# Kernel optimization log

Measured on AMD Instinct MI355X. Metric: run time of the kernel, lower is better.

Reference implementation:

```python
import jax, jax.numpy as jnp
import numpy as np

B, L, H, P, A, T = 64, 256, 1024, 64, 512, 8


def setup_inputs() -> dict:
    key = jax.random.key(0)
    ks = jax.random.split(key, 9)
    return {
        "word_hiddens": jax.random.normal(ks[0], (B, L, H), dtype=jnp.float32),
        "pos_e1_embeddings": jax.random.normal(ks[1], (B, L, P), dtype=jnp.float32),
        "pos_e2_embeddings": jax.random.normal(ks[2], (B, L, P), dtype=jnp.float32),
        "e1_end": jax.random.randint(ks[3], (B,), 0, L, dtype=jnp.int32),
        "e2_end": jax.random.randint(ks[4], (B,), 0, L, dtype=jnp.int32),
        "type_embeddings": jax.random.normal(ks[5], (T, H), dtype=jnp.float32) * 0.03,
        "W_pos": jax.random.normal(ks[6], (H + 2 * P, A), dtype=jnp.float32) * 0.03,
        "W_ent": jax.random.normal(ks[7], (4 * H, A), dtype=jnp.float32) * 0.02,
        "v": jax.random.normal(ks[8], (A,), dtype=jnp.float32) * 0.05,
    }


def _latent_type(e_h, type_emb):
    # alpha = softmax(e_h @ C^T); latent type = alpha @ C   (C: [T, latent])
    scores = jnp.einsum("bh,th->bt", e_h, type_emb)
    alpha = jax.nn.softmax(scores, axis=-1)
    return jnp.einsum("bt,th->bh", alpha, type_emb)


def reference(word_hiddens, pos_e1_embeddings, pos_e2_embeddings, e1_end, e2_end,
              type_embeddings, W_pos, W_ent, v):
    b, seq_len, h = word_hiddens.shape
    batch_idx = jnp.arange(b)
    e1_h = word_hiddens[batch_idx, e1_end]          # [B, H]
    e2_h = word_hiddens[batch_idx, e2_end]          # [B, H]
    e1_type = _latent_type(e1_h, type_embeddings)   # [B, H]
    e2_type = _latent_type(e2_h, type_embeddings)   # [B, H]

    entity_features = jnp.concatenate([e1_h, e1_type, e2_h, e2_type], axis=-1)  # [B, 4H]
    pos_features = jnp.concatenate([word_hiddens, pos_e1_embeddings, pos_e2_embeddings], axis=-1)  # [B, L, H+2P]

    dense_pos = jnp.einsum("blf,fa->bla", pos_features, W_pos)   # [B, L, A]
    dense_ent = entity_features @ W_ent                          # [B, A]
    # Faithful to original tf.repeat(axis=1)+reshape (element-interleaved, not a broadcast)
    dense_ent_r = jnp.repeat(dense_ent, seq_len, axis=1).reshape(b, seq_len, -1)  # [B, L, A]

    u = jnp.tanh(dense_pos + dense_ent_r)            # [B, L, A]
    vu = jnp.einsum("bla,a->bl", u, v)               # [B, L]
    alpha = jax.nn.softmax(vu, axis=-1)              # [B, L]
    z = jnp.einsum("blh,bl->bh", word_hiddens, alpha)  # [B, H]
    return z
```

## Files before the change

### kernel.cpp

```cpp
#include <hip/hip_runtime.h>
#include <hip/hip_bf16.h>
#include <math.h>

#define B_ 64
#define L_ 256
#define H_ 1024
#define P_ 64
#define A_ 512
#define T_ 8
#define NSTEP 36

#define AS1 __attribute__((address_space(1)))
#define AS3 __attribute__((address_space(3)))

typedef __attribute__((ext_vector_type(8))) __bf16 bf16x8;
typedef __attribute__((ext_vector_type(4))) float f32x4;

__device__ __forceinline__ float bf2f(ushort u) {
  union { unsigned int i; float f; } v; v.i = ((unsigned int)u) << 16; return v.f;
}
__device__ __forceinline__ ushort f2bf_rne(float f) {
  union { float f; unsigned int i; } v; v.f = f;
  unsigned int r = v.i + 0x7FFFu + ((v.i >> 16) & 1u);
  return (ushort)(r >> 16);
}
__device__ __forceinline__ unsigned int pack2_rne(float a, float b) {
  return (unsigned int)f2bf_rne(a) | ((unsigned int)f2bf_rne(b) << 16);
}

template <bool BF16>
__device__ __forceinline__ float ld1(const void* p, size_t i) {
  if (BF16) return bf2f(((const ushort*)p)[i]);
  return ((const float*)p)[i];
}
template <bool BF16>
__device__ __forceinline__ float2 ld2(const void* p, size_t i) {
  if (BF16) {
    ushort2 u = *(const ushort2*)((const ushort*)p + i);
    return (float2){bf2f(u.x), bf2f(u.y)};
  }
  return *(const float2*)((const float*)p + i);
}
template <bool BF16>
__device__ __forceinline__ float4 ld4(const void* p, size_t i) {
  if (BF16) {
    ushort4 u = *(const ushort4*)((const ushort*)p + i);
    return (float4){bf2f(u.x), bf2f(u.y), bf2f(u.z), bf2f(u.w)};
  }
  return *(const float4*)((const float*)p + i);
}

__device__ __forceinline__ void gll16(const void* g, void* l) {
  __builtin_amdgcn_global_load_lds((const AS1 void*)g, (AS3 void*)l, 16, 0, 0);
}

__device__ __forceinline__ void bar_vm2() {
  __builtin_amdgcn_sched_barrier(0);
  asm volatile("s_waitcnt vmcnt(2) lgkmcnt(0)" ::: "memory");
  __builtin_amdgcn_sched_barrier(0);
  __builtin_amdgcn_s_barrier();
  __builtin_amdgcn_sched_barrier(0);
}
__device__ __forceinline__ void bar_vm0() {
  __builtin_amdgcn_sched_barrier(0);
  asm volatile("s_waitcnt vmcnt(0) lgkmcnt(0)" ::: "memory");
  __builtin_amdgcn_sched_barrier(0);
  __builtin_amdgcn_s_barrier();
  __builtin_amdgcn_sched_barrier(0);
}

template <bool BF16>
__global__ __launch_bounds__(256) void prep_k(
    const void* __restrict__ wpos, ushort* __restrict__ WTs,
    const void* __restrict__ wh, const int* __restrict__ e1e,
    const int* __restrict__ e2e, const void* __restrict__ temb,
    float* __restrict__ EF) {
  if (blockIdx.x < 576) {
    __shared__ ushort tile[32][33];
    const int s  = blockIdx.x >> 4;
    const int at = blockIdx.x & 15;
    const int tx = threadIdx.x & 31;
    const int ty = threadIdx.x >> 5;
#pragma unroll
    for (int i = 0; i < 4; ++i) {
      size_t idx = (size_t)(s * 32 + ty + i * 8) * A_ + at * 32 + tx;
      ushort u;
      if (BF16) u = ((const ushort*)wpos)[idx];
      else u = f2bf_rne(((const float*)wpos)[idx]);
      tile[ty + i * 8][tx] = u;
    }
    __syncthreads();
#pragma unroll
    for (int i = 0; i < 4; ++i) {
      WTs[(size_t)s * (A_ * 32) + (size_t)(at * 32 + ty + i * 8) * 32 + tx] =
          tile[tx][ty + i * 8];
    }
  } else {
    const int b = blockIdx.x - 576;
    const int tid = threadIdx.x;
    __shared__ float eh1[1024];
    __shared__ float eh2[1024];
    __shared__ float part[256][16];
    __shared__ float part2[16][17];
    __shared__ float scores[16];
    __shared__ float alpha[16];

    const size_t o1 = ((size_t)b * L_ + e1e[b]) * H_;
    const size_t o2 = ((size_t)b * L_ + e2e[b]) * H_;
    for (int h = tid; h < 1024; h += 256) {
      eh1[h] = ld1<BF16>(wh, o1 + h);
      eh2[h] = ld1<BF16>(wh, o2 + h);
    }
    __syncthreads();

    float p[16];
#pragma unroll
    for (int t = 0; t < 16; ++t) p[t] = 0.f;
    for (int h = tid; h < 1024; h += 256) {
      float a1 = eh1[h], a2 = eh2[h];
#pragma unroll
      for (int t = 0; t < 8; ++t) {
        float c = ld1<BF16>(temb, t * 1024 + h);
        p[t] += a1 * c;
        p[8 + t] += a2 * c;
      }
    }
#pragma unroll
    for (int t = 0; t < 16; ++t) part[tid][t] = p[t];
    __syncthreads();
    {
      const int t = tid & 15, j = tid >> 4;
      float s = 0.f;
#pragma unroll
      for (int i = 0; i < 16; ++i) s += part[j * 16 + i][t];
      part2[j][t] = s;
    }
    __syncthreads();
    if (tid < 16) {
      float s = 0.f;
#pragma unroll
      for (int i = 0; i < 16; ++i) s += part2[i][tid];
      scores[tid] = s;
    }
    __syncthreads();
    if (tid < 2) {
      const int base = tid * 8;
      float mx = scores[base];
      for (int t = 1; t < 8; ++t) mx = fmaxf(mx, scores[base + t]);
      float sum = 0.f;
      float e[8];
      for (int t = 0; t < 8; ++t) { e[t] = __expf(scores[base + t] - mx); sum += e[t]; }
      float inv = 1.f / sum;
      for (int t = 0; t < 8; ++t) alpha[base + t] = e[t] * inv;
    }
    __syncthreads();

    float* efb = EF + (size_t)b * 4096;
    for (int h = tid; h < 1024; h += 256) {
      float l1 = 0.f, l2 = 0.f;
#pragma unroll
      for (int t = 0; t < 8; ++t) {
        float c = ld1<BF16>(temb, t * 1024 + h);
        l1 += alpha[t] * c;
        l2 += alpha[8 + t] * c;
      }
      efb[h] = eh1[h];
      efb[1024 + h] = l1;
      efb[2048 + h] = eh2[h];
      efb[3072 + h] = l2;
    }
  }
}

template <bool BF16>
__global__ __launch_bounds__(256) void ent_gemm(const float* __restrict__ EF,
                                                const void* __restrict__ went,
                                                float* __restrict__ part) {
  const int mh = blockIdx.x & 1;
  const int nb = (blockIdx.x >> 1) & 3;
  const int kb = blockIdx.x >> 3;
  const int tid = threadIdx.x;
  __shared__ float efs[32][128];

  const int k0 = kb * 128;
  {
    const int kq = (tid & 31) * 4;
    for (int m = tid >> 5; m < 32; m += 8) {
      *(float4*)&efs[m][kq] = *(const float4*)&EF[(size_t)(mh * 32 + m) * 4096 + k0 + kq];
    }
  }
  __syncthreads();

  const int n0 = nb * 128 + (tid & 31) * 4;
  const int mg = (tid >> 5) * 4;
  float acc[4][4];
#pragma unroll
  for (int i = 0; i < 4; ++i)
#pragma unroll
    for (int j = 0; j < 4; ++j) acc[i][j] = 0.f;

  for (int k = 0; k < 128; ++k) {
    float4 w = ld4<BF16>(went, (size_t)(k0 + k) * A_ + n0);
#pragma unroll
    for (int i = 0; i < 4; ++i) {
      float e = efs[mg + i][k];
      acc[i][0] += e * w.x;
      acc[i][1] += e * w.y;
      acc[i][2] += e * w.z;
      acc[i][3] += e * w.w;
    }
  }
#pragma unroll
  for (int i = 0; i < 4; ++i) {
    *(float4*)&part[((size_t)kb * 64 + mh * 32 + mg + i) * A_ + n0] =
        (float4){acc[i][0], acc[i][1], acc[i][2], acc[i][3]};
  }
}

__global__ __launch_bounds__(256, 4) void fused_gemm_vu_bf16(
    const ushort* __restrict__ wh, const ushort* __restrict__ pe1,
    const ushort* __restrict__ pe2, const ushort* __restrict__ WTs,
    const float* __restrict__ part, const ushort* __restrict__ vvec,
    float* __restrict__ vu_part) {
  __shared__ __align__(16) ushort Abuf[2][2048];
  __shared__ __align__(16) ushort Bbuf[2][4096];
  __shared__ float vu_s[4][64];
  __shared__ float dense_s[64];

  const int tid = threadIdx.x;
  const int pid = blockIdx.x;
  const int wid = (pid & 7) * 128 + (pid >> 3);
  const int nb = wid & 3;
  const int mb = wid >> 2;
  const int rbase = mb * 64;
  const int wave = tid >> 6;
  const int lane = tid & 63;
  const int quad = lane >> 4;
  const int col = lane & 15;
  const int wr = wave >> 1;
  const int wc = wave & 1;

  int aoff[2], boff[4];
#pragma unroll
  for (int mf = 0; mf < 2; ++mf) {
    const int ra = wr * 32 + mf * 16 + col;
    aoff[mf] = ra * 32 + ((quad ^ ((ra >> 1) & 3)) << 3);
  }
#pragma unroll
  for (int nf = 0; nf < 4; ++nf) {
    const int rb = wc * 64 + nf * 16 + col;
    boff[nf] = rb * 32 + ((quad ^ ((rb >> 1) & 3)) << 3);
  }

  const int srow = tid >> 2;
  const int csw = (((tid & 3) ^ ((srow >> 1) & 3)) << 3);
  const ushort* aw  = wh  + (size_t)(rbase + srow) * H_ + csw;
  const ushort* ap1 = pe1 + (size_t)(rbase + srow) * P_ + csw;
  const ushort* ap2 = pe2 + (size_t)(rbase + srow) * P_ + csw;
  const ushort* b1  = WTs + (size_t)(nb * 128 + srow) * 32 + csw;
  const ushort* b2  = WTs + (size_t)(nb * 128 + 64 + srow) * 32 + csw;

  auto stage = [&](int buf, int s) {
    const ushort* as;
    if (s < 32)      as = aw + s * 32;
    else if (s < 34) as = ap1 + (s - 32) * 32;
    else             as = ap2 + (s - 34) * 32;
    const size_t so = (size_t)s * (A_ * 32);
    gll16(as, &Abuf[buf][wave * 512]);
    gll16(b1 + so, &Bbuf[buf][wave * 512]);
    gll16(b2 + so, &Bbuf[buf][2048 + wave * 512]);
  };

  f32x4 acc[2][4];
#pragma unroll
  for (int i = 0; i < 2; ++i)
#pragma unroll
    for (int j = 0; j < 4; ++j) acc[i][j] = (f32x4){0.f, 0.f, 0.f, 0.f};

  const int bidx = rbase >> 8;
  float de = 0.f;
  if (tid < 64) {
    const int a = 2 * ((rbase & 255) + tid) + (nb >> 1);
#pragma unroll
    for (int kb = 0; kb < 32; ++kb)
      de += part[((size_t)kb * 64 + bidx) * A_ + a];
  }
  stage(0, 0);
  if (tid < 64) dense_s[tid] = de;
  __syncthreads();

  int buf = 0;
  for (int s = 0; s < NSTEP; ++s) {
    if (s + 1 < NSTEP) stage(buf ^ 1, s + 1);
    const ushort* Ab = Abuf[buf];
    const ushort* Bb = Bbuf[buf];
    bf16x8 af[2], bfr[4];
#pragma unroll
    for (int mf = 0; mf < 2; ++mf) af[mf] = *(const bf16x8*)&Ab[aoff[mf]];
#pragma unroll
    for (int nf = 0; nf < 4; ++nf) bfr[nf] = *(const bf16x8*)&Bb[boff[nf]];
#pragma unroll
    for (int mf = 0; mf < 2; ++mf)
#pragma unroll
      for (int nf = 0; nf < 4; ++nf)
        acc[mf][nf] =
            __builtin_amdgcn_mfma_f32_16x16x32_bf16(af[mf], bfr[nf], acc[mf][nf], 0, 0, 0);
    __syncthreads();
    buf ^= 1;
  }

  float vv[4];
#pragma unroll
  for (int nf = 0; nf < 4; ++nf)
    vv[nf] = bf2f(vvec[nb * 128 + wc * 64 + nf * 16 + col]);

#pragma unroll
  for (int mf = 0; mf < 2; ++mf) {
    const int row0 = wr * 32 + mf * 16 + quad * 4;
    const float e0 = dense_s[row0 + 0];
    const float e1 = dense_s[row0 + 1];
    const float e2 = dense_s[row0 + 2];
    const float e3 = dense_s[row0 + 3];
    float s0 = 0.f, s1 = 0.f, s2 = 0.f, s3 = 0.f;
#pragma unroll
    for (int nf = 0; nf < 4; ++nf) {
      float vn = vv[nf];
      s0 += tanhf(acc[mf][nf][0] + e0) * vn;
      s1 += tanhf(acc[mf][nf][1] + e1) * vn;
      s2 += tanhf(acc[mf][nf][2] + e2) * vn;
      s3 += tanhf(acc[mf][nf][3] + e3) * vn;
    }
    s0 += __shfl_xor(s0, 1); s0 += __shfl_xor(s0, 2); s0 += __shfl_xor(s0, 4); s0 += __shfl_xor(s0, 8);
    s1 += __shfl_xor(s1, 1); s1 += __shfl_xor(s1, 2); s1 += __shfl_xor(s1, 4); s1 += __shfl_xor(s1, 8);
    s2 += __shfl_xor(s2, 1); s2 += __shfl_xor(s2, 2); s2 += __shfl_xor(s2, 4); s2 += __shfl_xor(s2, 8);
    s3 += __shfl_xor(s3, 1); s3 += __shfl_xor(s3, 2); s3 += __shfl_xor(s3, 4); s3 += __shfl_xor(s3, 8);
    if (col == 0) {
      vu_s[wave][row0 + 0] = s0;
      vu_s[wave][row0 + 1] = s1;
      vu_s[wave][row0 + 2] = s2;
      vu_s[wave][row0 + 3] = s3;
    }
  }
  __syncthreads();
  if (tid < 64) {
    const int wrr = tid >> 5;
    float s = vu_s[wrr * 2][tid] + vu_s[wrr * 2 + 1][tid];
    vu_part[(size_t)nb * (B_ * L_) + rbase + tid] = s;
  }
}

__global__ __launch_bounds__(256, 4) void fused_gemm_vu_f32(
    const float* __restrict__ wh, const float* __restrict__ pe1,
    const float* __restrict__ pe2, const ushort* __restrict__ WTs,
    const float* __restrict__ part, const float* __restrict__ vvec,
    float* __restrict__ vu_part) {
  __shared__ __align__(16) ushort Abuf[2][2048];
  __shared__ __align__(16) ushort Bbuf[2][4096];
  __shared__ float vu_s[4][64];
  __shared__ float dense_s[64];

  const int tid = threadIdx.x;
  const int pid = blockIdx.x;
  const int wid = (pid & 7) * 128 + (pid >> 3);
  const int nb = wid & 3;
  const int mb = wid >> 2;
  const int rbase = mb * 64;
  const int wave = tid >> 6;
  const int lane = tid & 63;
  const int quad = lane >> 4;
  const int col = lane & 15;
  const int wr = wave >> 1;
  const int wc = wave & 1;

  int aoff[2], boff[4];
#pragma unroll
  for (int mf = 0; mf < 2; ++mf) {
    const int ra = wr * 32 + mf * 16 + col;
    aoff[mf] = ra * 32 + ((quad ^ ((ra >> 1) & 3)) << 3);
  }
#pragma unroll
  for (int nf = 0; nf < 4; ++nf) {
    const int rb = wc * 64 + nf * 16 + col;
    boff[nf] = rb * 32 + ((quad ^ ((rb >> 1) & 3)) << 3);
  }

  const int srow = tid >> 2;
  const int csw = (((tid & 3) ^ ((srow >> 1) & 3)) << 3);
  const ushort* b1 = WTs + (size_t)(nb * 128 + srow) * 32 + csw;
  const ushort* b2 = WTs + (size_t)(nb * 128 + 64 + srow) * 32 + csw;
  auto gllB = [&](int buf, int s) {
    const size_t so = (size_t)s * (A_ * 32);
    gll16(b1 + so, &Bbuf[buf][wave * 512]);
    gll16(b2 + so, &Bbuf[buf][2048 + wave * 512]);
  };

  const int ar0 = tid >> 2, aq = tid & 3;
  const int sA0 = ar0 * 32 + ((aq ^ ((ar0 >> 1) & 3)) << 3);

  f32x4 acc[2][4];
#pragma unroll
  for (int i = 0; i < 2; ++i)
#pragma unroll
    for (int j = 0; j < 4; ++j) acc[i][j] = (f32x4){0.f, 0.f, 0.f, 0.f};

  float4 fXa, fXb;
  float4 fYa, fYb;

  auto ISSUE_X = [&](int s) {
    const float* src; int ld, k0;
    if (s < 32)      { src = wh;  ld = H_; k0 = s * 32; }
    else if (s < 34) { src = pe1; ld = P_; k0 = (s - 32) * 32; }
    else             { src = pe2; ld = P_; k0 = (s - 34) * 32; }
    const float* p0 = src + (size_t)(rbase + ar0) * ld + k0 + aq * 8;
    fXa = *(const float4*)p0;
    fXb = *(const float4*)(p0 + 4);
  };
  auto ISSUE_Y = [&](int s) {
    const float* src; int ld, k0;
    if (s < 32)      { src = wh;  ld = H_; k0 = s * 32; }
    else if (s < 34) { src = pe1; ld = P_; k0 = (s - 32) * 32; }
    else             { src = pe2; ld = P_; k0 = (s - 34) * 32; }
    const float* p0 = src + (size_t)(rbase + ar0) * ld + k0 + aq * 8;
    fYa = *(const float4*)p0;
    fYb = *(const float4*)(p0 + 4);
  };
  auto STORE_X = [&](int buf) {
    uint4 u0 = {pack2_rne(fXa.x, fXa.y), pack2_rne(fXa.z, fXa.w),
                pack2_rne(fXb.x, fXb.y), pack2_rne(fXb.z, fXb.w)};
    *(uint4*)&Abuf[buf][sA0] = u0;
  };
  auto STORE_Y = [&](int buf) {
    uint4 u0 = {pack2_rne(fYa.x, fYa.y), pack2_rne(fYa.z, fYa.w),
                pack2_rne(fYb.x, fYb.y), pack2_rne(fYb.z, fYb.w)};
    *(uint4*)&Abuf[buf][sA0] = u0;
  };
  auto COMPUTE = [&](int buf) {
    bf16x8 af[2], bfr[4];
#pragma unroll
    for (int mf = 0; mf < 2; ++mf) af[mf] = *(const bf16x8*)&Abuf[buf][aoff[mf]];
#pragma unroll
    for (int nf = 0; nf < 4; ++nf) bfr[nf] = *(const bf16x8*)&Bbuf[buf][boff[nf]];
#pragma unroll
    for (int mf = 0; mf < 2; ++mf)
#pragma unroll
      for (int nf = 0; nf < 4; ++nf)
        acc[mf][nf] =
            __builtin_amdgcn_mfma_f32_16x16x32_bf16(af[mf], bfr[nf], acc[mf][nf], 0, 0, 0);
  };

  const int bidx = rbase >> 8;
  float de = 0.f;
  if (tid < 64) {
    const int a = 2 * ((rbase & 255) + tid) + (nb >> 1);
#pragma unroll
    for (int kb = 0; kb < 32; ++kb)
      de += part[((size_t)kb * 64 + bidx) * A_ + a];
  }
  gllB(0, 0);
  ISSUE_X(0);
  ISSUE_Y(1);
  STORE_X(0);
  if (tid < 64) dense_s[tid] = de;
  __syncthreads();

  for (int s = 0; s < NSTEP; s += 2) {
    gllB(1, s + 1);
    __builtin_amdgcn_sched_barrier(0);
    if (s + 2 < NSTEP) ISSUE_X(s + 2);
    COMPUTE(0);
    STORE_Y(1);
    if (s + 2 < NSTEP) bar_vm2(); else bar_vm0();
    if (s + 2 < NSTEP) {
      gllB(0, s + 2);
      __builtin_amdgcn_sched_barrier(0);
      if (s + 3 < NSTEP) ISSUE_Y(s + 3);
    }
    COMPUTE(1);
    if (s + 2 < NSTEP) {
      STORE_X(0);
      if (s + 3 < NSTEP) bar_vm2(); else bar_vm0();
    }
  }

  float vv[4];
#pragma unroll
  for (int nf = 0; nf < 4; ++nf)
    vv[nf] = vvec[nb * 128 + wc * 64 + nf * 16 + col];

#pragma unroll
  for (int mf = 0; mf < 2; ++mf) {
    const int row0 = wr * 32 + mf * 16 + quad * 4;
    const float e0 = dense_s[row0 + 0];
    const float e1 = dense_s[row0 + 1];
    const float e2 = dense_s[row0 + 2];
    const float e3 = dense_s[row0 + 3];
    float s0 = 0.f, s1 = 0.f, s2 = 0.f, s3 = 0.f;
#pragma unroll
    for (int nf = 0; nf < 4; ++nf) {
      float vn = vv[nf];
      s0 += tanhf(acc[mf][nf][0] + e0) * vn;
      s1 += tanhf(acc[mf][nf][1] + e1) * vn;
      s2 += tanhf(acc[mf][nf][2] + e2) * vn;
      s3 += tanhf(acc[mf][nf][3] + e3) * vn;
    }
    s0 += __shfl_xor(s0, 1); s0 += __shfl_xor(s0, 2); s0 += __shfl_xor(s0, 4); s0 += __shfl_xor(s0, 8);
    s1 += __shfl_xor(s1, 1); s1 += __shfl_xor(s1, 2); s1 += __shfl_xor(s1, 4); s1 += __shfl_xor(s1, 8);
    s2 += __shfl_xor(s2, 1); s2 += __shfl_xor(s2, 2); s2 += __shfl_xor(s2, 4); s2 += __shfl_xor(s2, 8);
    s3 += __shfl_xor(s3, 1); s3 += __shfl_xor(s3, 2); s3 += __shfl_xor(s3, 4); s3 += __shfl_xor(s3, 8);
    if (col == 0) {
      vu_s[wave][row0 + 0] = s0;
      vu_s[wave][row0 + 1] = s1;
      vu_s[wave][row0 + 2] = s2;
      vu_s[wave][row0 + 3] = s3;
    }
  }
  __syncthreads();
  if (tid < 64) {
    const int wrr = tid >> 5;
    float s = vu_s[wrr * 2][tid] + vu_s[wrr * 2 + 1][tid];
    vu_part[(size_t)nb * (B_ * L_) + rbase + tid] = s;
  }
}

template <bool BF16>
__global__ __launch_bounds__(256) void softmax_z(const void* __restrict__ wh,
                                                 const float* __restrict__ vu_part,
                                                 void* __restrict__ out) {
  const int b = blockIdx.x >> 1;
  const int hh = blockIdx.x & 1;
  const int tid = threadIdx.x;
  __shared__ float alpha[256];
  __shared__ float red[256];

  float x = 0.f;
#pragma unroll
  for (int p = 0; p < 4; ++p) x += vu_part[(size_t)p * (B_ * L_) + b * L_ + tid];
  red[tid] = x;
  __syncthreads();
  for (int s = 128; s > 0; s >>= 1) {
    if (tid < s) red[tid] = fmaxf(red[tid], red[tid + s]);
    __syncthreads();
  }
  float m = red[0];
  __syncthreads();
  float e = __expf(x - m);
  red[tid] = e;
  __syncthreads();
  for (int s = 128; s > 0; s >>= 1) {
    if (tid < s) red[tid] += red[tid + s];
    __syncthreads();
  }
  alpha[tid] = e / red[0];
  __syncthreads();

  const int h0 = hh * 512 + tid * 2;
  const size_t base = (size_t)b * L_ * H_ + h0;
  float z0 = 0.f, z1 = 0.f;
  for (int l = 0; l < 256; l += 8) {
    float2 u0 = ld2<BF16>(wh, base + (size_t)(l + 0) * H_);
    float2 u1 = ld2<BF16>(wh, base + (size_t)(l + 1) * H_);
    float2 u2 = ld2<BF16>(wh, base + (size_t)(l + 2) * H_);
    float2 u3 = ld2<BF16>(wh, base + (size_t)(l + 3) * H_);
    float2 u4 = ld2<BF16>(wh, base + (size_t)(l + 4) * H_);
    float2 u5 = ld2<BF16>(wh, base + (size_t)(l + 5) * H_);
    float2 u6 = ld2<BF16>(wh, base + (size_t)(l + 6) * H_);
    float2 u7 = ld2<BF16>(wh, base + (size_t)(l + 7) * H_);
    float a0 = alpha[l + 0], a1 = alpha[l + 1], a2 = alpha[l + 2], a3 = alpha[l + 3];
    float a4 = alpha[l + 4], a5 = alpha[l + 5], a6 = alpha[l + 6], a7 = alpha[l + 7];
    z0 += a0 * u0.x + a1 * u1.x + a2 * u2.x + a3 * u3.x
        + a4 * u4.x + a5 * u5.x + a6 * u6.x + a7 * u7.x;
    z1 += a0 * u0.y + a1 * u1.y + a2 * u2.y + a3 * u3.y
        + a4 * u4.y + a5 * u5.y + a6 * u6.y + a7 * u7.y;
  }
  if (BF16) {
    ((unsigned int*)out)[((size_t)b * H_ + h0) >> 1] = pack2_rne(z0, z1);
  } else {
    *(float2*)((float*)out + (size_t)b * H_ + h0) = (float2){z0, z1};
  }
}

extern "C" void kernel_launch(void* const* d_in, const int* in_sizes, int n_in,
                              void* d_out, int out_size, void* d_ws, size_t ws_size,
                              hipStream_t stream) {
  const void* wh   = d_in[0];
  const void* pe1  = d_in[1];
  const void* pe2  = d_in[2];
  const int*  e1e  = (const int*)d_in[3];
  const int*  e2e  = (const int*)d_in[4];
  const void* temb = d_in[5];
  const void* wpos = d_in[6];
  const void* went = d_in[7];
  const void* vvec = d_in[8];

  const bool bf16 = (in_sizes[0] == (int)(B_ * L_ * H_ * 2));

  char* ws = (char*)d_ws;
  ushort* WTs      = (ushort*)ws;
  float* vu_part   = (float*)(ws + 1310720);
  float* EF        = (float*)(ws + 1310720);
  float* part      = (float*)(ws + 2359296);

  if (bf16) {
    prep_k<true ><<<dim3(640), dim3(256), 0, stream>>>(wpos, WTs, wh, e1e, e2e, temb, EF);
    ent_gemm<true ><<<dim3(256), dim3(256), 0, stream>>>(EF, went, part);
    fused_gemm_vu_bf16<<<dim3(1024), dim3(256), 0, stream>>>(
        (const ushort*)wh, (const ushort*)pe1, (const ushort*)pe2, WTs, part,
        (const ushort*)vvec, vu_part);
    softmax_z<true ><<<dim3(128), dim3(256), 0, stream>>>(wh, vu_part, d_out);
  } else {
    prep_k<false><<<dim3(640), dim3(256), 0, stream>>>(wpos, WTs, wh, e1e, e2e, temb, EF);
    ent_gemm<false><<<dim3(256), dim3(256), 0, stream>>>(EF, went, part);
    fused_gemm_vu_f32<<<dim3(1024), dim3(256), 0, stream>>>(
        (const float*)wh, (const float*)pe1, (const float*)pe2, WTs, part,
        (const float*)vvec, vu_part);
    softmax_z<false><<<dim3(128), dim3(256), 0, stream>>>(wh, vu_part, d_out);
  }
}
```

Before: 187.1 us.

## Deepen fused GEMM pipeline to triple-buffered LDS with two-stage prefetch

Changes the fused GEMM + tanh/vu kernel's K-loop from double to triple buffering of the A and B LDS tiles. Global loads now run two stages ahead of compute, with vmcnt(6) waits in place of vmcnt(2). The aim is to hide more global memory latency behind the MFMA work. In exchange it uses more LDS and more registers for the extra prefetched A fragments, which could lower occupancy under the launch bound of 4 blocks.

```diff
diff --git a/kernel.cpp b/kernel.cpp
--- a/kernel.cpp
+++ b/kernel.cpp
@@ -54,19 +54,28 @@
   __builtin_amdgcn_global_load_lds((const AS1 void*)g, (AS3 void*)l, 16, 0, 0);
 }
 
-__device__ __forceinline__ void bar_vm2() {
-  __builtin_amdgcn_sched_barrier(0);
-  asm volatile("s_waitcnt vmcnt(2) lgkmcnt(0)" ::: "memory");
-  __builtin_amdgcn_sched_barrier(0);
+__device__ __forceinline__ void SB() { __builtin_amdgcn_sched_barrier(0); }
+
+__device__ __forceinline__ void bar_vm6() {
+  SB();
+  asm volatile("s_waitcnt vmcnt(6) lgkmcnt(0)" ::: "memory");
+  SB();
   __builtin_amdgcn_s_barrier();
-  __builtin_amdgcn_sched_barrier(0);
+  SB();
+}
+__device__ __forceinline__ void bar_vm4() {
+  SB();
+  asm volatile("s_waitcnt vmcnt(4) lgkmcnt(0)" ::: "memory");
+  SB();
+  __builtin_amdgcn_s_barrier();
+  SB();
 }
 __device__ __forceinline__ void bar_vm0() {
-  __builtin_amdgcn_sched_barrier(0);
+  SB();
   asm volatile("s_waitcnt vmcnt(0) lgkmcnt(0)" ::: "memory");
-  __builtin_amdgcn_sched_barrier(0);
+  SB();
   __builtin_amdgcn_s_barrier();
-  __builtin_amdgcn_sched_barrier(0);
+  SB();
 }
 
 template <bool BF16>
@@ -354,8 +363,8 @@
     const float* __restrict__ pe2, const ushort* __restrict__ WTs,
     const float* __restrict__ part, const float* __restrict__ vvec,
     float* __restrict__ vu_part) {
-  __shared__ __align__(16) ushort Abuf[2][2048];
-  __shared__ __align__(16) ushort Bbuf[2][4096];
+  __shared__ __align__(16) ushort Abuf[3][2048];
+  __shared__ __align__(16) ushort Bbuf[3][4096];
   __shared__ float vu_s[4][64];
   __shared__ float dense_s[64];
 
@@ -396,6 +405,35 @@
 
   const int ar0 = tid >> 2, aq = tid & 3;
   const int sA0 = ar0 * 32 + ((aq ^ ((ar0 >> 1) & 3)) << 3);
+  const float* asrc_w  = wh  + (size_t)(rbase + ar0) * H_ + aq * 8;
+  const float* asrc_p1 = pe1 + (size_t)(rbase + ar0) * P_ + aq * 8;
+  const float* asrc_p2 = pe2 + (size_t)(rbase + ar0) * P_ + aq * 8;
+
+  float4 fA0a, fA0b, fA1a, fA1b, fA2a, fA2b;
+
+  auto aptr = [&](int s) -> const float* {
+    if (s < 32) return asrc_w + s * 32;
+    if (s < 34) return asrc_p1 + (s - 32) * 32;
+    return asrc_p2 + (s - 34) * 32;
+  };
+  auto issue0 = [&](int s) { const float* p = aptr(s); fA0a = *(const float4*)p; fA0b = *(const float4*)(p + 4); };
+  auto issue1 = [&](int s) { const float* p = aptr(s); fA1a = *(const float4*)p; fA1b = *(const float4*)(p + 4); };
+  auto issue2 = [&](int s) { const float* p = aptr(s); fA2a = *(const float4*)p; fA2b = *(const float4*)(p + 4); };
+  auto store0 = [&](int buf) {
+    uint4 u = {pack2_rne(fA0a.x, fA0a.y), pack2_rne(fA0a.z, fA0a.w),
+               pack2_rne(fA0b.x, fA0b.y), pack2_rne(fA0b.z, fA0b.w)};
+    *(uint4*)&Abuf[buf][sA0] = u;
+  };
+  auto store1 = [&](int buf) {
+    uint4 u = {pack2_rne(fA1a.x, fA1a.y), pack2_rne(fA1a.z, fA1a.w),
+               pack2_rne(fA1b.x, fA1b.y), pack2_rne(fA1b.z, fA1b.w)};
+    *(uint4*)&Abuf[buf][sA0] = u;
+  };
+  auto store2 = [&](int buf) {
+    uint4 u = {pack2_rne(fA2a.x, fA2a.y), pack2_rne(fA2a.z, fA2a.w),
+               pack2_rne(fA2b.x, fA2b.y), pack2_rne(fA2b.z, fA2b.w)};
+    *(uint4*)&Abuf[buf][sA0] = u;
+  };
 
   f32x4 acc[2][4];
 #pragma unroll
@@ -403,37 +441,6 @@
 #pragma unroll
     for (int j = 0; j < 4; ++j) acc[i][j] = (f32x4){0.f, 0.f, 0.f, 0.f};
 
-  float4 fXa, fXb;
-  float4 fYa, fYb;
-
-  auto ISSUE_X = [&](int s) {
-    const float* src; int ld, k0;
-    if (s < 32)      { src = wh;  ld = H_; k0 = s * 32; }
-    else if (s < 34) { src = pe1; ld = P_; k0 = (s - 32) * 32; }
-    else             { src = pe2; ld = P_; k0 = (s - 34) * 32; }
-    const float* p0 = src + (size_t)(rbase + ar0) * ld + k0 + aq * 8;
-    fXa = *(const float4*)p0;
-    fXb = *(const float4*)(p0 + 4);
-  };
-  auto ISSUE_Y = [&](int s) {
-    const float* src; int ld, k0;
-    if (s < 32)      { src = wh;  ld = H_; k0 = s * 32; }
-    else if (s < 34) { src = pe1; ld = P_; k0 = (s - 32) * 32; }
-    else             { src = pe2; ld = P_; k0 = (s - 34) * 32; }
-    const float* p0 = src + (size_t)(rbase + ar0) * ld + k0 + aq * 8;
-    fYa = *(const float4*)p0;
-    fYb = *(const float4*)(p0 + 4);
-  };
-  auto STORE_X = [&](int buf) {
-    uint4 u0 = {pack2_rne(fXa.x, fXa.y), pack2_rne(fXa.z, fXa.w),
-                pack2_rne(fXb.x, fXb.y), pack2_rne(fXb.z, fXb.w)};
-    *(uint4*)&Abuf[buf][sA0] = u0;
-  };
-  auto STORE_Y = [&](int buf) {
-    uint4 u0 = {pack2_rne(fYa.x, fYa.y), pack2_rne(fYa.z, fYa.w),
-                pack2_rne(fYb.x, fYb.y), pack2_rne(fYb.z, fYb.w)};
-    *(uint4*)&Abuf[buf][sA0] = u0;
-  };
   auto COMPUTE = [&](int buf) {
     bf16x8 af[2], bfr[4];
 #pragma unroll
@@ -457,30 +464,41 @@
       de += part[((size_t)kb * 64 + bidx) * A_ + a];
   }
   gllB(0, 0);
-  ISSUE_X(0);
-  ISSUE_Y(1);
-  STORE_X(0);
+  gllB(1, 1);
+  SB();
+  issue0(0);
+  issue1(1);
+  issue2(2);
+  SB();
+  store0(0);
   if (tid < 64) dense_s[tid] = de;
-  __syncthreads();
-
-  for (int s = 0; s < NSTEP; s += 2) {
-    gllB(1, s + 1);
-    __builtin_amdgcn_sched_barrier(0);
-    if (s + 2 < NSTEP) ISSUE_X(s + 2);
+  bar_vm0();
+
+  for (int s = 0; s < 33; s += 3) {
+    gllB(2, s + 2); SB();
+    issue0(s + 3); SB();
     COMPUTE(0);
-    STORE_Y(1);
-    if (s + 2 < NSTEP) bar_vm2(); else bar_vm0();
-    if (s + 2 < NSTEP) {
-      gllB(0, s + 2);
-      __builtin_amdgcn_sched_barrier(0);
-      if (s + 3 < NSTEP) ISSUE_Y(s + 3);
-    }
+    store1(1);
+    bar_vm6();
+    gllB(0, s + 3); SB();
+    issue1(s + 4); SB();
     COMPUTE(1);
-    if (s + 2 < NSTEP) {
-      STORE_X(0);
-      if (s + 3 < NSTEP) bar_vm2(); else bar_vm0();
-    }
-  }
+    store2(2);
+    bar_vm6();
+    gllB(1, s + 4); SB();
+    issue2(s + 5); SB();
+    COMPUTE(2);
+    store0(0);
+    bar_vm6();
+  }
+  gllB(2, 35); SB();
+  COMPUTE(0);
+  store1(1);
+  bar_vm4();
+  COMPUTE(1);
+  store2(2);
+  bar_vm0();
+  COMPUTE(2);
 
   float vv[4];
 #pragma unroll
```

New measurement: 187.7 us. Within noise of the previous version (+0.4%).
